# Optimization experiments

Hardware: AMD Instinct MI355X
Metric: run time of the kernel (lower is better)

## Reference

```python
import jax, jax.numpy as jnp
import numpy as np

N = 40   # max_len (uniform sentence length)
B = 32   # batch
D = 768  # hidden size (bert-base)


def _ft(b, e, n):
    # flatten_tri from the original module
    L = e - b
    return (n + 1) * n // 2 - (n - L + 2) * (n - L + 1) // 2 + b


def setup_inputs() -> dict:
    key = jax.random.key(0)
    ks = jax.random.split(key, 4)
    base_vecs = jax.random.normal(ks[0], (N, B, D), jnp.float32)
    # xavier-ish scales so chart scores stay O(1)
    W_bil = jax.random.normal(ks[1], (D, D), jnp.float32) / D
    W1 = jax.random.normal(ks[2], (D, 2 * D), jnp.float32) / float(np.sqrt(2 * D))
    W2 = jax.random.normal(ks[3], (D, D), jnp.float32) / float(np.sqrt(D))
    b1 = jnp.zeros((D,), jnp.float32)
    b2 = jnp.zeros((D,), jnp.float32)
    root_bias = jnp.zeros((D,), jnp.float32)  # original init: zeros Parameter
    return {"base_vecs": base_vecs, "W_bil": W_bil, "W1": W1, "b1": b1,
            "W2": W2, "b2": b2, "root_bias": root_bias}


def reference(base_vecs, W_bil, W1, b1, W2, b2, root_bias):
    T = (N + 1) * N // 2
    relu = jax.nn.relu

    def compose(l, r):
        h = jnp.concatenate([l, r], axis=-1)          # [..., 2D]
        h = relu(h @ W1.T + b1)
        return relu(h @ W2.T + b2)                    # [..., D]

    def bil(l, r):
        return jnp.einsum('...d,de,...e->...', l, W_bil, r)[..., None]  # [..., 1]

    # ---- inside pass (bottom-up over span lengths, vectorized over begins) ----
    iv = jnp.zeros((T, B, D), base_vecs.dtype).at[:N].set(base_vecs)
    isc = jnp.zeros((T, B, 1), base_vecs.dtype)
    for L in range(2, N + 1):
        begins = range(N + 1 - L)
        il = jnp.asarray([[_ft(b, b + s, N) for s in range(1, L)] for b in begins])
        ir = jnp.asarray([[_ft(b + s, b + L, N) for s in range(1, L)] for b in begins])
        cell = jnp.asarray([_ft(b, b + L, N) for b in begins])
        l, r = iv[il], iv[ir]                          # [nb, L-1, B, D]
        sc = bil(l, r) + isc[il] + isc[ir]             # [nb, L-1, B, 1]
        v = compose(l, r)                              # [nb, L-1, B, D]
        w = jax.nn.softmax(sc, axis=1)                 # softmax over splits
        isc = isc.at[cell].set(jnp.sum(w * sc, axis=1))
        iv = iv.at[cell].set(jnp.sum(w * v, axis=1))

    # ---- outside pass (top-down). All sent_lengths == N => mask is all-zero. ----
    ov = jnp.zeros((T, B, D), base_vecs.dtype).at[_ft(0, N, N)].set(
        jnp.broadcast_to(root_bias, (B, D)))
    osc = jnp.zeros((T, B, 1), base_vecs.dtype)
    for L in range(N - 1, 0, -1):
        begins = range(N + 1 - L)
        ip = jnp.asarray([[_ft(c, b + L, N) for c in range(0, b)]
                          + [_ft(b, c, N) for c in range(b + L + 1, N + 1)]
                          for b in begins])             # [nb, N-L]
        is_ = jnp.asarray([[_ft(c, b, N) for c in range(0, b)]
                           + [_ft(b + L, c, N) for c in range(b + L + 1, N + 1)]
                           for b in begins])            # [nb, N-L]
        cell = jnp.asarray([_ft(b, b + L, N) for b in begins])
        p, s = ov[ip], iv[is_]                          # [nb, N-L, B, D]
        sc = bil(p, s) + osc[ip] + isc[is_]             # [nb, N-L, B, 1]
        v = compose(p, s)
        w = relu(jax.nn.softmax(sc, axis=1))            # relu is no-op here (mask==0)
        osc = osc.at[cell].set(jnp.sum(w * sc, axis=1))
        ov = ov.at[cell].set(jnp.sum(w * v, axis=1))

    # ---- reconstruction loss on terminals ----
    term = ov[:N]                                       # [N, B, D]
    num = jnp.sum(term * base_vecs, axis=2)
    den = jnp.maximum(jnp.linalg.norm(term, axis=2) * jnp.linalg.norm(base_vecs, axis=2), 1e-8)
    loss = jnp.sum(1.0 - num / den) / (N * B)
    return loss
```

## Files before the change

kernel.cpp:

```cpp
#include <hip/hip_runtime.h>
#include <math.h>

#define NN 40
#define DD 768
#define TT 820

typedef unsigned short u16;
typedef __attribute__((ext_vector_type(8))) short bfrag8;
typedef __attribute__((ext_vector_type(4))) float facc4;

__device__ __forceinline__ int ftd(int b, int e) {
    int l = e - b;
    return TT - (NN - l + 2) * (NN - l + 1) / 2 + b;
}
__device__ __forceinline__ float bf2f(u16 u) {
    union { unsigned int i; float f; } x; x.i = ((unsigned)u) << 16; return x.f;
}
__device__ __forceinline__ u16 f2bf(float f) {
    unsigned u = __float_as_uint(f);
    u += 0x7fff + ((u >> 16) & 1);
    return (u16)(u >> 16);
}
__device__ __forceinline__ unsigned cvtpk(float lo, float hi) {
    unsigned r;
    asm("v_cvt_pk_bf16_f32 %0, %1, %2" : "=v"(r) : "v"(lo), "v"(hi));
    return r;
}
__device__ __forceinline__ float dot2(unsigned a, unsigned c) {
    return bf2f((u16)a) * bf2f((u16)c) + bf2f((u16)(a >> 16)) * bf2f((u16)(c >> 16));
}

#define GLOAD16(gp, lp) __builtin_amdgcn_global_load_lds( \
    (const __attribute__((address_space(1))) unsigned int*)(gp), \
    (__attribute__((address_space(3))) unsigned int*)(lp), 16, 0, 0)

#define MODE_IN 1
#define MODE_OUT 2


template<int MODE>
__device__ __forceinline__ void pairmap(int r, int g0, int Sps, int level,
                                        int& uc, int& vc, int& bb)
{
    int p = r >> 5; bb = r & 31;
    int g = g0 + p / Sps, si = p % Sps;
    if (MODE == MODE_IN) {
        int s = si + 1;
        uc = ftd(g, g + s); vc = ftd(g + s, g + level);
    } else {
        if (si < g) { uc = ftd(si, g + level); vc = ftd(si, g); }
        else { int c = si + level + 1; uc = ftd(g, c); vc = ftd(g + level, c); }
    }
}

__global__ __launch_bounds__(256)
void transform_k(const u16* __restrict__ A, const u16* __restrict__ Wcat,
                 u16* __restrict__ OutU, u16* __restrict__ OutV,
                 u16* __restrict__ OutW, const float* __restrict__ bias, int M)
{
    __shared__ __align__(16) u16 As[64 * 32];
    __shared__ __align__(16) u16 Bs[128 * 32];
    const int tid = threadIdx.x, lane = tid & 63, wv = tid >> 6;
    const int m0 = blockIdx.x * 64;
    const int slab = blockIdx.y / 6;
    const int j0 = (blockIdx.y % 6) * 128;
    u16* Out = (slab == 0) ? OutU : (slab == 1 ? OutV : OutW);

    const int srow = tid >> 2;
    const int kos = (((tid & 3) ^ ((tid >> 3) & 3))) * 8;
    int ar = m0 + srow; if (ar >= M) ar = M - 1;
    const u16* ap = A + (size_t)ar * DD + kos;
    const u16* bq0 = Wcat + (size_t)(slab * DD + j0 + srow) * DD + kos;
    const u16* bq1 = bq0 + (size_t)64 * DD;
    u16* AsW  = As + wv * 512;
    u16* BsW0 = Bs + wv * 512;  u16* BsW1 = Bs + 2048 + wv * 512;

    facc4 acc[2][4];
    #pragma unroll
    for (int i = 0; i < 2; ++i)
        #pragma unroll
        for (int j = 0; j < 4; ++j) acc[i][j] = (facc4){0.f, 0.f, 0.f, 0.f};

    const int wr = wv >> 1, wc = wv & 1;
    const int fr = lane & 15;
    const int sk = ((lane >> 4) ^ ((lane >> 1) & 3)) * 8;

    for (int k0 = 0; k0 < DD; k0 += 32) {
        GLOAD16(ap + k0, AsW);
        GLOAD16(bq0 + k0, BsW0);
        GLOAD16(bq1 + k0, BsW1);
        __syncthreads();
        bfrag8 a[2], b[4];
        #pragma unroll
        for (int fi = 0; fi < 2; ++fi)
            a[fi] = *(const bfrag8*)&As[(wr * 32 + fi * 16 + fr) * 32 + sk];
        #pragma unroll
        for (int fj = 0; fj < 4; ++fj)
            b[fj] = *(const bfrag8*)&Bs[(wc * 64 + fj * 16 + fr) * 32 + sk];
        #pragma unroll
        for (int fi = 0; fi < 2; ++fi)
            #pragma unroll
            for (int fj = 0; fj < 4; ++fj)
                acc[fi][fj] = __builtin_amdgcn_mfma_f32_16x16x32_bf16(
                    a[fi], b[fj], acc[fi][fj], 0, 0, 0);
        __syncthreads();
    }

    const int r0l = (lane >> 4) * 4;
    #pragma unroll
    for (int fi = 0; fi < 2; ++fi)
        #pragma unroll
        for (int r = 0; r < 4; ++r) {
            int m = m0 + wr * 32 + fi * 16 + r0l + r;
            if (m < M) {
                #pragma unroll
                for (int fj = 0; fj < 4; ++fj) {
                    int n = j0 + wc * 64 + fj * 16 + fr;
                    float vo = acc[fi][fj][r];
                    if (slab == 1) vo += bias[n];
                    Out[(size_t)m * DD + n] = f2bf(vo);
                }
            }
        }
}

template<int MODE>
__global__ __launch_bounds__(512)
void gemm2f_k(const u16* __restrict__ Ubase, const u16* __restrict__ Vbase,
              const u16* __restrict__ W2, const float* __restrict__ b2,
              const float* __restrict__ wbuf, u16* __restrict__ Out,
              int M, int level, int g0, int Sps)
{
    const int q = blockIdx.x;
    const int cxcd = q & 7, tq = q >> 3;
    const int mblk = (tq / 3) * 8 + cxcd;
    const int jt = tq % 3;
    const int m0 = mblk * 128;
    if (m0 >= M) return;
    const int j0 = jt * 256;

    __shared__ __align__(16) u16 As[2][128 * 32];
    __shared__ __align__(16) u16 Bs[2][256 * 32];
    const int tid = threadIdx.x, lane = tid & 63, wv = tid >> 6;

    const int srow = tid >> 2;
    const int ko = (tid & 3) * 8;
    const int aslot = ((tid & 3) ^ ((tid >> 3) & 3)) * 8;
    const int NT = DD / 32;

    const u16 *u0, *v0;
    {
        int r = m0 + srow; if (r >= M) r = M - 1;
        int uc, vc, bb;
        pairmap<MODE>(r, g0, Sps, level, uc, vc, bb);
        u0 = Ubase + (size_t)(uc * 32 + bb) * DD + ko;
        v0 = Vbase + (size_t)(vc * 32 + bb) * DD + ko;
    }

    const int ksrc = ((lane & 3) ^ ((lane >> 3) & 3)) * 8;
    const int brow0 = wv * 16 + (lane >> 2);
    const u16* bsrc0 = W2 + (size_t)(j0 + brow0) * DD + ksrc;
    const u16* bsrc1 = W2 + (size_t)(j0 + 128 + brow0) * DD + ksrc;
    const int bofs0 = wv * 512;
    const int bofs1 = 4096 + wv * 512;

    facc4 acc[4][4];
    #pragma unroll
    for (int i = 0; i < 4; ++i)
        #pragma unroll
        for (int j = 0; j < 4; ++j) acc[i][j] = (facc4){0.f, 0.f, 0.f, 0.f};

    const int wr = wv >> 2, wc = wv & 3;
    const int fr = lane & 15;
    const int sk = ((lane >> 4) ^ ((lane >> 1) & 3)) * 8;

    GLOAD16(bsrc0, &Bs[0][bofs0]);
    GLOAD16(bsrc1, &Bs[0][bofs1]);
    bfrag8 uc_ = *(const bfrag8*)(u0);
    bfrag8 vc_ = *(const bfrag8*)(v0);
    {
        float f[8];
        #pragma unroll
        for (int j = 0; j < 8; ++j)
            f[j] = fmaxf(bf2f((u16)uc_[j]) + bf2f((u16)vc_[j]), 0.f);
        uint4 pk;
        pk.x = cvtpk(f[0], f[1]); pk.y = cvtpk(f[2], f[3]);
        pk.z = cvtpk(f[4], f[5]); pk.w = cvtpk(f[6], f[7]);
        *(uint4*)&As[0][srow * 32 + aslot] = pk;
    }
    bfrag8 un_ = *(const bfrag8*)(u0 + 32);
    bfrag8 vn_ = *(const bfrag8*)(v0 + 32);
    __syncthreads();

    for (int t = 0; t < NT; ++t) {
        const int cur = t & 1;
        if (t + 1 < NT) {
            GLOAD16(bsrc0 + (t + 1) * 32, &Bs[cur ^ 1][bofs0]);
            GLOAD16(bsrc1 + (t + 1) * 32, &Bs[cur ^ 1][bofs1]);
            float f[8];
            #pragma unroll
            for (int j = 0; j < 8; ++j)
                f[j] = fmaxf(bf2f((u16)un_[j]) + bf2f((u16)vn_[j]), 0.f);
            uint4 pk;
            pk.x = cvtpk(f[0], f[1]); pk.y = cvtpk(f[2], f[3]);
            pk.z = cvtpk(f[4], f[5]); pk.w = cvtpk(f[6], f[7]);
            *(uint4*)&As[cur ^ 1][srow * 32 + aslot] = pk;
            if (t + 2 < NT) {
                un_ = *(const bfrag8*)(u0 + (t + 2) * 32);
                vn_ = *(const bfrag8*)(v0 + (t + 2) * 32);
            }
        }
        bfrag8 a[4], b[4];
        #pragma unroll
        for (int fi = 0; fi < 4; ++fi)
            a[fi] = *(const bfrag8*)&As[cur][(wr * 64 + fi * 16 + fr) * 32 + sk];
        #pragma unroll
        for (int fj = 0; fj < 4; ++fj)
            b[fj] = *(const bfrag8*)&Bs[cur][(wc * 64 + fj * 16 + fr) * 32 + sk];
        #pragma unroll
        for (int fi = 0; fi < 4; ++fi)
            #pragma unroll
            for (int fj = 0; fj < 4; ++fj)
                acc[fi][fj] = __builtin_amdgcn_mfma_f32_16x16x32_bf16(
                    a[fi], b[fj], acc[fi][fj], 0, 0, 0);
        __syncthreads();
    }

    const int r0l = (lane >> 4) * 4;
    #pragma unroll
    for (int fi = 0; fi < 4; ++fi)
        #pragma unroll
        for (int r = 0; r < 4; ++r) {
            int m = m0 + wr * 64 + fi * 16 + r0l + r;
            if (m < M) {
                float wt = wbuf[m];
                #pragma unroll
                for (int fj = 0; fj < 4; ++fj) {
                    int n = j0 + wc * 64 + fj * 16 + fr;
                    float v = fmaxf(acc[fi][fj][r] + b2[n], 0.f) * wt;
                    Out[(size_t)m * DD + n] = f2bf(v);
                }
            }
        }
}

__global__ __launch_bounds__(256)
void reduce_k(const u16* __restrict__ v, u16* __restrict__ chart,
              int cellrow0, int rows, int Sps)
{
    int idx = blockIdx.x * 256 + threadIdx.x;
    int tot = rows * 96;
    if (idx >= tot) return;
    int row = idx / 96, c8 = (idx % 96) * 8;
    int gl = row >> 5, bb = row & 31;
    const u16* p = v + ((size_t)(gl * Sps) * 32 + bb) * DD + c8;
    const size_t st = (size_t)32 * DD;
    float a0[8] = {}, a1[8] = {}, a2[8] = {}, a3[8] = {};
    int s = 0;
    for (; s + 4 <= Sps; s += 4) {
        bfrag8 x0 = *(const bfrag8*)(p + (size_t)(s + 0) * st);
        bfrag8 x1 = *(const bfrag8*)(p + (size_t)(s + 1) * st);
        bfrag8 x2 = *(const bfrag8*)(p + (size_t)(s + 2) * st);
        bfrag8 x3 = *(const bfrag8*)(p + (size_t)(s + 3) * st);
        #pragma unroll
        for (int j = 0; j < 8; ++j) {
            a0[j] += bf2f((u16)x0[j]);
            a1[j] += bf2f((u16)x1[j]);
            a2[j] += bf2f((u16)x2[j]);
            a3[j] += bf2f((u16)x3[j]);
        }
    }
    for (; s < Sps; ++s) {
        bfrag8 x = *(const bfrag8*)(p + (size_t)s * st);
        #pragma unroll
        for (int j = 0; j < 8; ++j) a0[j] += bf2f((u16)x[j]);
    }
    #pragma unroll
    for (int j = 0; j < 8; ++j) a0[j] += (a1[j] + a2[j]) + a3[j];
    uint4 pk;
    pk.x = cvtpk(a0[0], a0[1]); pk.y = cvtpk(a0[2], a0[3]);
    pk.z = cvtpk(a0[4], a0[5]); pk.w = cvtpk(a0[6], a0[7]);
    *(uint4*)&chart[(size_t)(cellrow0 + row) * DD + c8] = pk;
}

template<bool INSIDE>
__global__ __launch_bounds__(512)
void scoresm_k(const u16* __restrict__ ivb, const u16* __restrict__ IWb,
               const u16* __restrict__ ovb, float* __restrict__ isc,
               float* __restrict__ osc, float* __restrict__ wbuf,
               int level, int Sps, int cellrow0)
{
    __shared__ float sS[40];
    const int blk = blockIdx.x;
    const int gl = blk >> 5, bb = blk & 31;
    const int lane = threadIdx.x & 63, wv = threadIdx.x >> 6;

    for (int s = wv; s < Sps; s += 8) {
        const u16 *lp, *rp; float add;
        if (INSIDE) {
            int lc = ftd(gl, gl + s + 1), rc = ftd(gl + s + 1, gl + level);
            lp = ivb + (size_t)(lc * 32 + bb) * DD;
            rp = IWb + (size_t)(rc * 32 + bb) * DD;
            add = isc[lc * 32 + bb] + isc[rc * 32 + bb];
        } else {
            int pc, scl;
            if (s < gl) { pc = ftd(s, gl + level); scl = ftd(s, gl); }
            else { int c2 = s + level + 1; pc = ftd(gl, c2); scl = ftd(gl + level, c2); }
            lp = ovb + (size_t)(pc * 32 + bb) * DD;
            rp = IWb + (size_t)(scl * 32 + bb) * DD;
            add = osc[pc * 32 + bb] + isc[scl * 32 + bb];
        }
        float sum = 0.f;
        #pragma unroll
        for (int i = 0; i < 3; ++i) {
            uint2 a = *(const uint2*)(lp + i * 256 + lane * 4);
            uint2 c = *(const uint2*)(rp + i * 256 + lane * 4);
            sum += dot2(a.x, c.x) + dot2(a.y, c.y);
        }
        #pragma unroll
        for (int off = 32; off; off >>= 1) sum += __shfl_xor(sum, off);
        if (lane == 0) sS[s] = sum + add;
    }
    __syncthreads();
    if (wv == 0) {
        bool act = lane < Sps;
        float x = act ? sS[lane] : -3.0e38f;
        float m = x;
        #pragma unroll
        for (int off = 32; off; off >>= 1) m = fmaxf(m, __shfl_xor(m, off));
        float e = act ? expf(x - m) : 0.f;
        float ssum = e;
        #pragma unroll
        for (int off = 32; off; off >>= 1) ssum += __shfl_xor(ssum, off);
        float wt = e / ssum;
        if (act) wbuf[(gl * Sps + lane) * 32 + bb] = wt;
        float ws = act ? wt * x : 0.f;
        #pragma unroll
        for (int off = 32; off; off >>= 1) ws += __shfl_xor(ws, off);
        if (lane == 0) {
            float* scout = INSIDE ? isc : osc;
            scout[cellrow0 + gl * 32 + bb] = ws;
        }
    }
}

__global__ __launch_bounds__(256)
void loss_part(const u16* __restrict__ ovb, const float* __restrict__ base,
               float* __restrict__ lb)
{
    int wid = (blockIdx.x * 256 + threadIdx.x) >> 6;
    int lane = threadIdx.x & 63;
    if (wid >= NN * 32) return;
    const u16* t = ovb + (size_t)wid * DD;
    const float* b = base + (size_t)wid * DD;
    float num = 0, nt = 0, nb = 0;
    #pragma unroll
    for (int i = 0; i < 3; ++i) {
        uint2 a2 = *(const uint2*)(t + i * 256 + lane * 4);
        float4 c = *(const float4*)(b + i * 256 + lane * 4);
        float a0 = bf2f((u16)a2.x), a1 = bf2f((u16)(a2.x >> 16));
        float a2f = bf2f((u16)a2.y), a3 = bf2f((u16)(a2.y >> 16));
        num += a0 * c.x + a1 * c.y + a2f * c.z + a3 * c.w;
        nt  += a0 * a0 + a1 * a1 + a2f * a2f + a3 * a3;
        nb  += c.x * c.x + c.y * c.y + c.z * c.z + c.w * c.w;
    }
    #pragma unroll
    for (int off = 32; off; off >>= 1) {
        num += __shfl_down(num, off);
        nt  += __shfl_down(nt, off);
        nb  += __shfl_down(nb, off);
    }
    if (lane == 0) {
        float den = fmaxf(sqrtf(nt) * sqrtf(nb), 1e-8f);
        lb[wid] = 1.f - num / den;
    }
}

__global__ void loss_fin(const float* __restrict__ lb, float* __restrict__ out)
{
    __shared__ float red[256];
    float s = 0;
    for (int i = threadIdx.x; i < NN * 32; i += 256) s += lb[i];
    red[threadIdx.x] = s;
    __syncthreads();
    for (int o = 128; o; o >>= 1) {
        if (threadIdx.x < o) red[threadIdx.x] += red[threadIdx.x + o];
        __syncthreads();
    }
    if (threadIdx.x == 0) out[0] = red[0] / (NN * 32.f);
}

__global__ void build_wcat(const float* __restrict__ W1, const float* __restrict__ Wbil,
                           u16* __restrict__ Wcat)
{
    int idx = blockIdx.x * 256 + threadIdx.x;
    if (idx >= 2304 * DD) return;
    int r = idx / DD, k = idx % DD;
    float v;
    if (r < 768) v = W1[(size_t)r * 1536 + k];
    else if (r < 1536) v = W1[(size_t)(r - 768) * 1536 + 768 + k];
    else v = Wbil[(size_t)(r - 1536) * DD + k];
    Wcat[idx] = f2bf(v);
}

__global__ void cvt_k(const float* __restrict__ in, u16* __restrict__ out, int n)
{
    int idx = blockIdx.x * 256 + threadIdx.x;
    if (idx < n) out[idx] = f2bf(in[idx]);
}

__global__ void init_rootb(u16* __restrict__ ovb, const float* __restrict__ rb)
{
    int idx = blockIdx.x * 256 + threadIdx.x;
    if (idx < 32 * DD) ovb[(size_t)819 * 32 * DD + idx] = f2bf(rb[idx % DD]);
}

extern "C" void kernel_launch(void* const* d_in, const int* in_sizes, int n_in,
                              void* d_out, int out_size, void* d_ws, size_t ws_size,
                              hipStream_t stream)
{
    const float* base  = (const float*)d_in[0];
    const float* Wbil  = (const float*)d_in[1];
    const float* W1    = (const float*)d_in[2];
    const float* b1    = (const float*)d_in[3];
    const float* W2    = (const float*)d_in[4];
    const float* b2    = (const float*)d_in[5];
    const float* rbias = (const float*)d_in[6];
    float* out = (float*)d_out;

    char* ws = (char*)d_ws;
    size_t off = 0;
    auto alloc = [&](size_t bytes) { size_t o = off; off = (off + bytes + 255) & ~(size_t)255; return o; };
    const size_t SB = (size_t)TT * 32 * DD * 2;
    u16*  ivb = (u16*)(ws + alloc(SB));
    u16*  ovb = (u16*)(ws + alloc(SB));
    u16*  Ub  = (u16*)(ws + alloc(SB));
    u16*  Vb  = (u16*)(ws + alloc(SB));
    u16*  IWb = (u16*)(ws + alloc(SB));
    u16*  Wcat = (u16*)(ws + alloc((size_t)2304 * DD * 2));
    u16*  W2b  = (u16*)(ws + alloc((size_t)DD * DD * 2));
    float* isc = (float*)(ws + alloc((size_t)TT * 32 * 4));
    float* osc = (float*)(ws + alloc((size_t)TT * 32 * 4));
    float* wb  = (float*)(ws + alloc((size_t)1560 * 32 * 4));
    float* lb  = (float*)(ws + alloc((size_t)NN * 32 * 4));
    u16* vin = (u16*)(ws + off);
    size_t vbytes = (ws_size > off) ? (ws_size - off) : 0;

    hipMemsetAsync(isc, 0, (size_t)TT * 32 * 4, stream);
    hipMemsetAsync(osc, 0, (size_t)TT * 32 * 4, stream);
    build_wcat<<<(2304 * DD + 255) / 256, 256, 0, stream>>>(W1, Wbil, Wcat);
    cvt_k<<<(DD * DD + 255) / 256, 256, 0, stream>>>(W2, W2b, DD * DD);
    cvt_k<<<(NN * 32 * DD + 255) / 256, 256, 0, stream>>>(base, ivb, NN * 32 * DD);
    init_rootb<<<(32 * DD + 255) / 256, 256, 0, stream>>>(ovb, rbias);
    {
        int M = NN * 32;
        dim3 g((M + 63) / 64, 18);
        transform_k<<<g, 256, 0, stream>>>(ivb, Wcat, Ub, Vb, IWb, b1, M);
    }

    auto g2grid = [](int Mc) {
        int xb = (Mc + 127) / 128;
        int XB8 = ((xb + 7) / 8) * 8;
        return 3 * XB8;
    };

    for (int L = 2; L <= NN - 1; ++L) {
        int S = L - 1, nb = NN + 1 - L;
        int cellbase = TT - (NN - L + 2) * (NN - L + 1) / 2;
        scoresm_k<true><<<nb * 32, 512, 0, stream>>>(
            ivb, IWb, ovb, isc, osc, wb, L, S, cellbase * 32);
        size_t perbegin = (size_t)S * 32 * DD * 2;
        int GC = (vbytes >= perbegin) ? (int)(vbytes / perbegin) : 1;
        if (GC < 1) GC = 1;
        if (GC > nb) GC = nb;
        for (int g0 = 0; g0 < nb; g0 += GC) {
            int gc = (g0 + GC <= nb) ? GC : (nb - g0);
            int Mc = gc * S * 32;
            u16* vout = (S == 1) ? (ivb + (size_t)(cellbase + g0) * 32 * DD) : vin;
            gemm2f_k<MODE_IN><<<g2grid(Mc), 512, 0, stream>>>(
                Ub, Vb, W2b, b2, wb + (size_t)g0 * S * 32, vout, Mc, L, g0, S);
            if (S > 1)
                reduce_k<<<(gc * 32 * 96 + 255) / 256, 256, 0, stream>>>(
                    vin, ivb, (cellbase + g0) * 32, gc * 32, S);
        }
        {
            int M = nb * 32;
            dim3 g((M + 63) / 64, 18);
            transform_k<<<g, 256, 0, stream>>>(
                ivb + (size_t)cellbase * 32 * DD, Wcat,
                Ub + (size_t)cellbase * 32 * DD, Vb + (size_t)cellbase * 32 * DD,
                IWb + (size_t)cellbase * 32 * DD, b1, M);
        }
    }

    {
        dim3 g(1, 6);
        transform_k<<<g, 256, 0, stream>>>(
            ovb + (size_t)819 * 32 * DD, Wcat,
            Ub + (size_t)819 * 32 * DD, nullptr, nullptr, b1, 32);
    }

    for (int L = NN - 1; L >= 1; --L) {
        int S = NN - L, nb = NN + 1 - L;
        int cellbase = TT - (NN - L + 2) * (NN - L + 1) / 2;
        scoresm_k<false><<<nb * 32, 512, 0, stream>>>(
            ivb, IWb, ovb, isc, osc, wb, L, S, cellbase * 32);
        size_t perbegin = (size_t)S * 32 * DD * 2;
        int GC = (vbytes >= perbegin) ? (int)(vbytes / perbegin) : 1;
        if (GC < 1) GC = 1;
        if (GC > nb) GC = nb;
        for (int g0 = 0; g0 < nb; g0 += GC) {
            int gc = (g0 + GC <= nb) ? GC : (nb - g0);
            int Mc = gc * S * 32;
            u16* vout = (S == 1) ? (ovb + (size_t)(cellbase + g0) * 32 * DD) : vin;
            gemm2f_k<MODE_OUT><<<g2grid(Mc), 512, 0, stream>>>(
                Ub, Vb, W2b, b2, wb + (size_t)g0 * S * 32, vout, Mc, L, g0, S);
            if (S > 1)
                reduce_k<<<(gc * 32 * 96 + 255) / 256, 256, 0, stream>>>(
                    vin, ovb, (cellbase + g0) * 32, gc * 32, S);
        }
        if (L > 1) {
            int M = nb * 32;
            dim3 g((M + 63) / 64, 6);
            transform_k<<<g, 256, 0, stream>>>(
                ovb + (size_t)cellbase * 32 * DD, Wcat,
                Ub + (size_t)cellbase * 32 * DD, nullptr, nullptr, b1, M);
        }
    }

    loss_part<<<(NN * 32 + 3) / 4, 256, 0, stream>>>(ovb, base, lb);
    loss_fin<<<1, 256, 0, stream>>>(lb, out);
}
```

Before: 5.146 ms.

## Fuse split-score softmax into GEMM launch and apply weights in reduction

The separate bilinear-score/softmax kernel is folded into the GEMM kernel as extra trailing blocks, launched only with the first chunk of each level. This removes one kernel launch per level. Because the softmax weights now come from blocks running in the same launch, the GEMM epilogue no longer multiplies by them. The reduction kernel applies the weights instead, which keeps the data dependency correct but adds weight loads to the reduce step. The S==1 case relies on the softmax weight being exactly 1.

```diff
diff --git a/kernel.cpp b/kernel.cpp
--- a/kernel.cpp
+++ b/kernel.cpp
@@ -36,7 +36,6 @@
 
 #define MODE_IN 1
 #define MODE_OUT 2
-
 
 template<int MODE>
 __device__ __forceinline__ void pairmap(int r, int g0, int Sps, int level,
@@ -126,11 +125,71 @@
 
 template<int MODE>
 __global__ __launch_bounds__(512)
-void gemm2f_k(const u16* __restrict__ Ubase, const u16* __restrict__ Vbase,
-              const u16* __restrict__ W2, const float* __restrict__ b2,
-              const float* __restrict__ wbuf, u16* __restrict__ Out,
-              int M, int level, int g0, int Sps)
-{
+void level_k(const u16* __restrict__ Ubase, const u16* __restrict__ Vbase,
+             const u16* __restrict__ W2, const float* __restrict__ b2,
+             u16* __restrict__ Out, int M, int level, int g0, int Sps, int NG,
+             const u16* __restrict__ ivb, const u16* __restrict__ IWb,
+             const u16* __restrict__ ovb, float* __restrict__ isc,
+             float* __restrict__ osc, float* __restrict__ wbuf, int cellrow0)
+{
+    __shared__ __align__(16) u16 As[2][128 * 32];
+    __shared__ __align__(16) u16 Bs[2][256 * 32];
+    const int tid = threadIdx.x, lane = tid & 63, wv = tid >> 6;
+
+    if (blockIdx.x >= NG) {
+        float* sS = (float*)&As[0][0];
+        const int blk = blockIdx.x - NG;
+        const int gl = blk >> 5, bb = blk & 31;
+        for (int s = wv; s < Sps; s += 8) {
+            const u16 *lp, *rp; float add;
+            if (MODE == MODE_IN) {
+                int lc = ftd(gl, gl + s + 1), rc = ftd(gl + s + 1, gl + level);
+                lp = ivb + (size_t)(lc * 32 + bb) * DD;
+                rp = IWb + (size_t)(rc * 32 + bb) * DD;
+                add = isc[lc * 32 + bb] + isc[rc * 32 + bb];
+            } else {
+                int pc, scl;
+                if (s < gl) { pc = ftd(s, gl + level); scl = ftd(s, gl); }
+                else { int c2 = s + level + 1; pc = ftd(gl, c2); scl = ftd(gl + level, c2); }
+                lp = ovb + (size_t)(pc * 32 + bb) * DD;
+                rp = IWb + (size_t)(scl * 32 + bb) * DD;
+                add = osc[pc * 32 + bb] + isc[scl * 32 + bb];
+            }
+            float sum = 0.f;
+            #pragma unroll
+            for (int i = 0; i < 3; ++i) {
+                uint2 a = *(const uint2*)(lp + i * 256 + lane * 4);
+                uint2 c = *(const uint2*)(rp + i * 256 + lane * 4);
+                sum += dot2(a.x, c.x) + dot2(a.y, c.y);
+            }
+            #pragma unroll
+            for (int off = 32; off; off >>= 1) sum += __shfl_xor(sum, off);
+            if (lane == 0) sS[s] = sum + add;
+        }
+        __syncthreads();
+        if (wv == 0) {
+            bool act = lane < Sps;
+            float x = act ? sS[lane] : -3.0e38f;
+            float m = x;
+            #pragma unroll
+            for (int off = 32; off; off >>= 1) m = fmaxf(m, __shfl_xor(m, off));
+            float e = act ? expf(x - m) : 0.f;
+            float ssum = e;
+            #pragma unroll
+            for (int off = 32; off; off >>= 1) ssum += __shfl_xor(ssum, off);
+            float wt = e / ssum;
+            if (act) wbuf[(gl * Sps + lane) * 32 + bb] = wt;
+            float ws = act ? wt * x : 0.f;
+            #pragma unroll
+            for (int off = 32; off; off >>= 1) ws += __shfl_xor(ws, off);
+            if (lane == 0) {
+                float* scout = (MODE == MODE_IN) ? isc : osc;
+                scout[cellrow0 + gl * 32 + bb] = ws;
+            }
+        }
+        return;
+    }
+
     const int q = blockIdx.x;
     const int cxcd = q & 7, tq = q >> 3;
     const int mblk = (tq / 3) * 8 + cxcd;
@@ -138,10 +197,6 @@
     const int m0 = mblk * 128;
     if (m0 >= M) return;
     const int j0 = jt * 256;
-
-    __shared__ __align__(16) u16 As[2][128 * 32];
-    __shared__ __align__(16) u16 Bs[2][256 * 32];
-    const int tid = threadIdx.x, lane = tid & 63, wv = tid >> 6;
 
     const int srow = tid >> 2;
     const int ko = (tid & 3) * 8;
@@ -233,11 +288,10 @@
         for (int r = 0; r < 4; ++r) {
             int m = m0 + wr * 64 + fi * 16 + r0l + r;
             if (m < M) {
-                float wt = wbuf[m];
                 #pragma unroll
                 for (int fj = 0; fj < 4; ++fj) {
                     int n = j0 + wc * 64 + fj * 16 + fr;
-                    float v = fmaxf(acc[fi][fj][r] + b2[n], 0.f) * wt;
+                    float v = fmaxf(acc[fi][fj][r] + b2[n], 0.f);
                     Out[(size_t)m * DD + n] = f2bf(v);
                 }
             }
@@ -245,8 +299,8 @@
 }
 
 __global__ __launch_bounds__(256)
-void reduce_k(const u16* __restrict__ v, u16* __restrict__ chart,
-              int cellrow0, int rows, int Sps)
+void reduce_k(const u16* __restrict__ v, const float* __restrict__ wbuf,
+              u16* __restrict__ chart, int cellrow0, int rows, int Sps)
 {
     int idx = blockIdx.x * 256 + threadIdx.x;
     int tot = rows * 96;
@@ -254,6 +308,7 @@
     int row = idx / 96, c8 = (idx % 96) * 8;
     int gl = row >> 5, bb = row & 31;
     const u16* p = v + ((size_t)(gl * Sps) * 32 + bb) * DD + c8;
+    const float* wp = wbuf + (size_t)gl * Sps * 32 + bb;
     const size_t st = (size_t)32 * DD;
     float a0[8] = {}, a1[8] = {}, a2[8] = {}, a3[8] = {};
     int s = 0;
@@ -262,18 +317,23 @@
         bfrag8 x1 = *(const bfrag8*)(p + (size_t)(s + 1) * st);
         bfrag8 x2 = *(const bfrag8*)(p + (size_t)(s + 2) * st);
         bfrag8 x3 = *(const bfrag8*)(p + (size_t)(s + 3) * st);
+        float w0 = wp[(size_t)(s + 0) * 32];
+        float w1 = wp[(size_t)(s + 1) * 32];
+        float w2 = wp[(size_t)(s + 2) * 32];
+        float w3 = wp[(size_t)(s + 3) * 32];
         #pragma unroll
         for (int j = 0; j < 8; ++j) {
-            a0[j] += bf2f((u16)x0[j]);
-            a1[j] += bf2f((u16)x1[j]);
-            a2[j] += bf2f((u16)x2[j]);
-            a3[j] += bf2f((u16)x3[j]);
+            a0[j] += w0 * bf2f((u16)x0[j]);
+            a1[j] += w1 * bf2f((u16)x1[j]);
+            a2[j] += w2 * bf2f((u16)x2[j]);
+            a3[j] += w3 * bf2f((u16)x3[j]);
         }
     }
     for (; s < Sps; ++s) {
         bfrag8 x = *(const bfrag8*)(p + (size_t)s * st);
-        #pragma unroll
-        for (int j = 0; j < 8; ++j) a0[j] += bf2f((u16)x[j]);
+        float w = wp[(size_t)s * 32];
+        #pragma unroll
+        for (int j = 0; j < 8; ++j) a0[j] += w * bf2f((u16)x[j]);
     }
     #pragma unroll
     for (int j = 0; j < 8; ++j) a0[j] += (a1[j] + a2[j]) + a3[j];
@@ -281,67 +341,6 @@
     pk.x = cvtpk(a0[0], a0[1]); pk.y = cvtpk(a0[2], a0[3]);
     pk.z = cvtpk(a0[4], a0[5]); pk.w = cvtpk(a0[6], a0[7]);
     *(uint4*)&chart[(size_t)(cellrow0 + row) * DD + c8] = pk;
-}
-
-template<bool INSIDE>
-__global__ __launch_bounds__(512)
-void scoresm_k(const u16* __restrict__ ivb, const u16* __restrict__ IWb,
-               const u16* __restrict__ ovb, float* __restrict__ isc,
-               float* __restrict__ osc, float* __restrict__ wbuf,
-               int level, int Sps, int cellrow0)
-{
-    __shared__ float sS[40];
-    const int blk = blockIdx.x;
-    const int gl = blk >> 5, bb = blk & 31;
-    const int lane = threadIdx.x & 63, wv = threadIdx.x >> 6;
-
-    for (int s = wv; s < Sps; s += 8) {
-        const u16 *lp, *rp; float add;
-        if (INSIDE) {
-            int lc = ftd(gl, gl + s + 1), rc = ftd(gl + s + 1, gl + level);
-            lp = ivb + (size_t)(lc * 32 + bb) * DD;
-            rp = IWb + (size_t)(rc * 32 + bb) * DD;
-            add = isc[lc * 32 + bb] + isc[rc * 32 + bb];
-        } else {
-            int pc, scl;
-            if (s < gl) { pc = ftd(s, gl + level); scl = ftd(s, gl); }
-            else { int c2 = s + level + 1; pc = ftd(gl, c2); scl = ftd(gl + level, c2); }
-            lp = ovb + (size_t)(pc * 32 + bb) * DD;
-            rp = IWb + (size_t)(scl * 32 + bb) * DD;
-            add = osc[pc * 32 + bb] + isc[scl * 32 + bb];
-        }
-        float sum = 0.f;
-        #pragma unroll
-        for (int i = 0; i < 3; ++i) {
-            uint2 a = *(const uint2*)(lp + i * 256 + lane * 4);
-            uint2 c = *(const uint2*)(rp + i * 256 + lane * 4);
-            sum += dot2(a.x, c.x) + dot2(a.y, c.y);
-        }
-        #pragma unroll
-        for (int off = 32; off; off >>= 1) sum += __shfl_xor(sum, off);
-        if (lane == 0) sS[s] = sum + add;
-    }
-    __syncthreads();
-    if (wv == 0) {
-        bool act = lane < Sps;
-        float x = act ? sS[lane] : -3.0e38f;
-        float m = x;
-        #pragma unroll
-        for (int off = 32; off; off >>= 1) m = fmaxf(m, __shfl_xor(m, off));
-        float e = act ? expf(x - m) : 0.f;
-        float ssum = e;
-        #pragma unroll
-        for (int off = 32; off; off >>= 1) ssum += __shfl_xor(ssum, off);
-        float wt = e / ssum;
-        if (act) wbuf[(gl * Sps + lane) * 32 + bb] = wt;
-        float ws = act ? wt * x : 0.f;
-        #pragma unroll
-        for (int off = 32; off; off >>= 1) ws += __shfl_xor(ws, off);
-        if (lane == 0) {
-            float* scout = INSIDE ? isc : osc;
-            scout[cellrow0 + gl * 32 + bb] = ws;
-        }
-    }
 }
 
 __global__ __launch_bounds__(256)
@@ -467,8 +466,6 @@
     for (int L = 2; L <= NN - 1; ++L) {
         int S = L - 1, nb = NN + 1 - L;
         int cellbase = TT - (NN - L + 2) * (NN - L + 1) / 2;
-        scoresm_k<true><<<nb * 32, 512, 0, stream>>>(
-            ivb, IWb, ovb, isc, osc, wb, L, S, cellbase * 32);
         size_t perbegin = (size_t)S * 32 * DD * 2;
         int GC = (vbytes >= perbegin) ? (int)(vbytes / perbegin) : 1;
         if (GC < 1) GC = 1;
@@ -477,11 +474,14 @@
             int gc = (g0 + GC <= nb) ? GC : (nb - g0);
             int Mc = gc * S * 32;
             u16* vout = (S == 1) ? (ivb + (size_t)(cellbase + g0) * 32 * DD) : vin;
-            gemm2f_k<MODE_IN><<<g2grid(Mc), 512, 0, stream>>>(
-                Ub, Vb, W2b, b2, wb + (size_t)g0 * S * 32, vout, Mc, L, g0, S);
+            int NG = g2grid(Mc);
+            int nblk = NG + ((g0 == 0) ? nb * 32 : 0);
+            level_k<MODE_IN><<<nblk, 512, 0, stream>>>(
+                Ub, Vb, W2b, b2, vout, Mc, L, g0, S, NG,
+                ivb, IWb, ovb, isc, osc, wb, cellbase * 32);
             if (S > 1)
                 reduce_k<<<(gc * 32 * 96 + 255) / 256, 256, 0, stream>>>(
-                    vin, ivb, (cellbase + g0) * 32, gc * 32, S);
+                    vin, wb + (size_t)g0 * S * 32, ivb, (cellbase + g0) * 32, gc * 32, S);
         }
         {
             int M = nb * 32;
@@ -503,8 +503,6 @@
     for (int L = NN - 1; L >= 1; --L) {
         int S = NN - L, nb = NN + 1 - L;
         int cellbase = TT - (NN - L + 2) * (NN - L + 1) / 2;
-        scoresm_k<false><<<nb * 32, 512, 0, stream>>>(
-            ivb, IWb, ovb, isc, osc, wb, L, S, cellbase * 32);
         size_t perbegin = (size_t)S * 32 * DD * 2;
         int GC = (vbytes >= perbegin) ? (int)(vbytes / perbegin) : 1;
         if (GC < 1) GC = 1;
@@ -513,11 +511,14 @@
             int gc = (g0 + GC <= nb) ? GC : (nb - g0);
             int Mc = gc * S * 32;
             u16* vout = (S == 1) ? (ovb + (size_t)(cellbase + g0) * 32 * DD) : vin;
-            gemm2f_k<MODE_OUT><<<g2grid(Mc), 512, 0, stream>>>(
-                Ub, Vb, W2b, b2, wb + (size_t)g0 * S * 32, vout, Mc, L, g0, S);
+            int NG = g2grid(Mc);
+            int nblk = NG + ((g0 == 0) ? nb * 32 : 0);
+            level_k<MODE_OUT><<<nblk, 512, 0, stream>>>(
+                Ub, Vb, W2b, b2, vout, Mc, L, g0, S, NG,
+                ivb, IWb, ovb, isc, osc, wb, cellbase * 32);
             if (S > 1)
                 reduce_k<<<(gc * 32 * 96 + 255) / 256, 256, 0, stream>>>(
-                    vin, ovb, (cellbase + g0) * 32, gc * 32, S);
+                    vin, wb + (size_t)g0 * S * 32, ovb, (cellbase + g0) * 32, gc * 32, S);
         }
         if (L > 1) {
             int M = nb * 32;
```

Result: faster. 4.666 ms, median of 2 (-9.3%).
